# Optimization experiments

Measured on AMD Instinct MI355X. Metric: run time of the kernel, lower is better.

## Reference

```python
import jax, jax.numpy as jnp
import numpy as np

B, S, D = 4, 2048, 1024
LN_EPS = 1e-3  # keras LayerNormalization default


def setup_inputs() -> dict:
    key = jax.random.key(0)
    ks = jax.random.split(key, 4)
    std = 1.0 / np.sqrt(D)
    return {
        "inputs": jax.random.normal(ks[0], (B, S, D), dtype=jnp.float32),
        "Wq": jax.random.normal(ks[1], (D, D), dtype=jnp.float32) * std,
        "bq": jnp.zeros((D,), jnp.float32),
        "Wk": jax.random.normal(ks[2], (D, D), dtype=jnp.float32) * std,
        "bk": jnp.zeros((D,), jnp.float32),
        "Wv": jax.random.normal(ks[3], (D, D), dtype=jnp.float32) * std,
        "bv": jnp.zeros((D,), jnp.float32),
        "ln_gamma": jnp.ones((D,), jnp.float32),
        "ln_beta": jnp.zeros((D,), jnp.float32),
    }


def reference(inputs, Wq, bq, Wk, bk, Wv, bv, ln_gamma, ln_beta):
    d = inputs.shape[-1]
    scale = jnp.sqrt(jnp.asarray(d, inputs.dtype))
    q = inputs @ Wq + bq          # [B,S,D]
    k = inputs @ Wk + bk
    v = inputs @ Wv + bv
    scores = jnp.einsum("bqd,bkd->bqk", q, k) / scale  # [B,S,S]
    attn = jax.nn.softmax(scores, axis=-1)
    context = jnp.einsum("bqk,bkd->bqd", attn, v)      # [B,S,D]
    resid = context + inputs
    mu = jnp.mean(resid, axis=-1, keepdims=True)
    var = jnp.mean(jnp.square(resid - mu), axis=-1, keepdims=True)
    normed = (resid - mu) * jax.lax.rsqrt(var + LN_EPS)
    return normed * ln_gamma + ln_beta
```

## Files before the change

### kernel.cpp

```cpp
#include <hip/hip_runtime.h>
#include <hip/hip_bf16.h>
#include <cstdint>
#include <cstddef>


typedef unsigned short u16;
using bf16x8 = __attribute__((ext_vector_type(8))) short;
using f32x16 = __attribute__((ext_vector_type(16))) float;

typedef __attribute__((address_space(3))) unsigned int lds_uint;
typedef const __attribute__((address_space(1))) unsigned int glob_uint;

__device__ __forceinline__ float bf2f(u16 h) {
    union { unsigned int u; float f; } c;
    c.u = ((unsigned int)h) << 16;
    return c.f;
}
__device__ __forceinline__ u16 f2bf(float f) {
    union { float f; unsigned int u; } c;
    c.f = f;
    return (u16)((c.u + 0x7fffu + ((c.u >> 16) & 1u)) >> 16);
}
__device__ __forceinline__ void load_lds16(const void* g, void* l) {
    __builtin_amdgcn_global_load_lds((glob_uint*)g, (lds_uint*)l, 16, 0, 0);
}

__device__ __forceinline__ int detect_fp32(const u16* X, int* sflag) {
    const int t = threadIdx.x;
    if (t < 64) {
        bool bad = false, nz = false;
#pragma unroll
        for (int j = 0; j < 4; ++j) {
            float v = bf2f(X[(t * 4 + j) * 2]);
            if (!(fabsf(v) <= 1e9f)) bad = true;
            if (v != 0.f) nz = true;
        }
        unsigned long long ab = __ballot(bad);
        unsigned long long an = __ballot(nz);
        if (t == 0) *sflag = (ab != 0ull || an == 0ull) ? 1 : 0;
    }
    __syncthreads();
    return *sflag;
}

__global__ __launch_bounds__(256) void prep_kernel(
    const void* __restrict__ X, const void* __restrict__ Wq,
    const void* __restrict__ Wk, const void* __restrict__ Wv,
    const void* __restrict__ bq, const void* __restrict__ bk,
    const void* __restrict__ bv, const void* __restrict__ gamma,
    const void* __restrict__ beta,
    u16* __restrict__ Xb, u16* __restrict__ Wt, u16* __restrict__ bias5)
{
    __shared__ u16 tile[64][72];
    __shared__ int sflag;
    const int fp32 = detect_fp32((const u16*)X, &sflag);
    const int t   = threadIdx.x;
    const int blk = blockIdx.x;

    if (blk < 4096) {
        const size_t i = ((size_t)blk * 256 + t) * 8;
        if (fp32) {
            const float* f = (const float*)X;
            float4 a = *(const float4*)(f + i);
            float4 b = *(const float4*)(f + i + 4);
            ushort4 o0, o1;
            o0.x = f2bf(a.x); o0.y = f2bf(a.y); o0.z = f2bf(a.z); o0.w = f2bf(a.w);
            o1.x = f2bf(b.x); o1.y = f2bf(b.y); o1.z = f2bf(b.z); o1.w = f2bf(b.w);
            *(ushort4*)(Xb + i) = o0;
            *(ushort4*)(Xb + i + 4) = o1;
        } else {
            *(uint4*)(Xb + i) = *(const uint4*)((const u16*)X + i);
        }
    } else if (blk < 4864) {
        const int idx = blk - 4096;
        const int k0 = (idx & 15) * 64;
        const int n0 = ((idx >> 4) & 15) * 64;
        const int w  = idx >> 8;
        const void* W = (w == 0) ? Wq : ((w == 1) ? Wk : Wv);
#pragma unroll
        for (int it = 0; it < 2; ++it) {
            int i2 = t + it * 256;
            int r = i2 >> 3;
            int c = (i2 & 7) * 8;
            const size_t off = (size_t)(k0 + r) * 1024 + n0 + c;
            if (fp32) {
                const float* Wf = (const float*)W + off;
                float4 a = *(const float4*)Wf;
                float4 b = *(const float4*)(Wf + 4);
                u16* tp = &tile[r][c];
                tp[0] = f2bf(a.x); tp[1] = f2bf(a.y); tp[2] = f2bf(a.z); tp[3] = f2bf(a.w);
                tp[4] = f2bf(b.x); tp[5] = f2bf(b.y); tp[6] = f2bf(b.z); tp[7] = f2bf(b.w);
            } else {
                *(uint4*)&tile[r][c] = *(const uint4*)((const u16*)W + off);
            }
        }
        __syncthreads();
#pragma unroll
        for (int it = 0; it < 2; ++it) {
            int i2 = t + it * 256;
            int r = i2 >> 3;
            int c = (i2 & 7) * 8;
            union { u16 s[8]; uint4 v; } tmp;
#pragma unroll
            for (int j = 0; j < 8; ++j) tmp.s[j] = tile[c + j][r];
            *(uint4*)(Wt + (size_t)(w * 1024 + n0 + r) * 1024 + k0 + c) = tmp.v;
        }
    } else {
        const int v = blk - 4864;
        const void* srcs[5] = {bq, bk, bv, gamma, beta};
        const void* src = srcs[v];
        u16* d = bias5 + (size_t)v * 1024;
        const int i = t * 4;
        if (fp32) {
            const float* f = (const float*)src;
            ushort4 o;
            o.x = f2bf(f[i]); o.y = f2bf(f[i + 1]);
            o.z = f2bf(f[i + 2]); o.w = f2bf(f[i + 3]);
            *(ushort4*)(d + i) = o;
        } else {
            *(ushort4*)(d + i) = *(const ushort4*)((const u16*)src + i);
        }
    }
}

__global__ __launch_bounds__(256) void proj_kernel(
    const u16* __restrict__ Xb, const u16* __restrict__ Wt,
    u16* __restrict__ QK2, u16* __restrict__ Vt, const u16* __restrict__ bias5)
{
    __shared__ u16 As[2][128 * 32];
    __shared__ u16 Bs[2][128 * 32];
    const int id   = blockIdx.x;
    const bool vt  = (id >= 1024);
    const u16* A;  const u16* Bt;  u16* C;
    int lda, ldb, ldc, m0, n0;
    if (!vt) {
        A = Xb;  lda = 1024;  Bt = Wt;  ldb = 1024;  C = QK2;  ldc = 2048;
        n0 = (id & 15) * 128;  m0 = (id >> 4) * 128;
    } else {
        const int i2 = id - 1024;
        A = Wt + (size_t)2 * 1024 * 1024;  lda = 1024;
        Bt = Xb;  ldb = 1024;  C = Vt;  ldc = 8192;
        n0 = (i2 & 63) * 128;  m0 = (i2 >> 6) * 128;
    }
    const int t    = threadIdx.x;
    const int lane = t & 63;
    const int w    = t >> 6;
    const int wr   = w >> 1, wc = w & 1;

    const int srow = lane >> 2;
    const int skg  = (lane & 3) ^ ((srow >> 1) & 3);
    const u16* Ag0 = A  + (size_t)(m0 + w * 32 +      srow) * lda + skg * 8;
    const u16* Ag1 = A  + (size_t)(m0 + w * 32 + 16 + srow) * lda + skg * 8;
    const u16* Bg0 = Bt + (size_t)(n0 + w * 32 +      srow) * ldb + skg * 8;
    const u16* Bg1 = Bt + (size_t)(n0 + w * 32 + 16 + srow) * ldb + skg * 8;
    u16* Al0 = &As[0][(w * 32) * 32];
    u16* Al1 = &As[1][(w * 32) * 32];
    u16* Bl0 = &Bs[0][(w * 32) * 32];
    u16* Bl1 = &Bs[1][(w * 32) * 32];

    f32x16 acc[2][2];
#pragma unroll
    for (int mi = 0; mi < 2; ++mi)
#pragma unroll
        for (int ni = 0; ni < 2; ++ni)
#pragma unroll
            for (int r = 0; r < 16; ++r)
                acc[mi][ni][r] = 0.f;

    const int ml  = lane & 31;
    const int kh  = lane >> 5;
    const int key = (ml >> 1) & 3;

    for (int k0 = 0; k0 < 1024; k0 += 64) {
        load_lds16(Ag0 + k0,      Al0);
        load_lds16(Ag1 + k0,      Al0 + 16 * 32);
        load_lds16(Bg0 + k0,      Bl0);
        load_lds16(Bg1 + k0,      Bl0 + 16 * 32);
        load_lds16(Ag0 + k0 + 32, Al1);
        load_lds16(Ag1 + k0 + 32, Al1 + 16 * 32);
        load_lds16(Bg0 + k0 + 32, Bl1);
        load_lds16(Bg1 + k0 + 32, Bl1 + 16 * 32);
        __syncthreads();
#pragma unroll
        for (int slab = 0; slab < 2; ++slab) {
            const u16* as_ = As[slab];
            const u16* bs_ = Bs[slab];
#pragma unroll
            for (int s = 0; s < 2; ++s) {
                const int g    = s * 2 + kh;
                const int slot = (g ^ key) * 8;
                bf16x8 a0 = *(const bf16x8*)&as_[(wr * 64 +      ml) * 32 + slot];
                bf16x8 a1 = *(const bf16x8*)&as_[(wr * 64 + 32 + ml) * 32 + slot];
                bf16x8 b0 = *(const bf16x8*)&bs_[(wc * 64 +      ml) * 32 + slot];
                bf16x8 b1 = *(const bf16x8*)&bs_[(wc * 64 + 32 + ml) * 32 + slot];
                acc[0][0] = __builtin_amdgcn_mfma_f32_32x32x16_bf16(a0, b0, acc[0][0], 0, 0, 0);
                acc[0][1] = __builtin_amdgcn_mfma_f32_32x32x16_bf16(a0, b1, acc[0][1], 0, 0, 0);
                acc[1][0] = __builtin_amdgcn_mfma_f32_32x32x16_bf16(a1, b0, acc[1][0], 0, 0, 0);
                acc[1][1] = __builtin_amdgcn_mfma_f32_32x32x16_bf16(a1, b1, acc[1][1], 0, 0, 0);
            }
        }
        __syncthreads();
    }

    const int colb = n0 + wc * 64 + ml;
    const int rowb = m0 + wr * 64 + 4 * kh;
#pragma unroll
    for (int mi = 0; mi < 2; ++mi) {
#pragma unroll
        for (int ni = 0; ni < 2; ++ni) {
            const int col = colb + ni * 32;
            const float cbias = vt ? 0.f : bf2f(bias5[col]);
#pragma unroll
            for (int r = 0; r < 16; ++r) {
                const int row = rowb + mi * 32 + (r & 3) + 8 * (r >> 2);
                const float bias = vt ? bf2f(bias5[2048 + row]) : cbias;
                C[(size_t)row * ldc + col] = f2bf(acc[mi][ni][r] + bias);
            }
        }
    }
}

template<int EPI, int KSPLIT>
__global__ __launch_bounds__(512, 2) void gemm256r(
    const u16* __restrict__ A, int lda, size_t sA,
    const u16* __restrict__ Bt, int ldb, size_t sB,
    u16* __restrict__ C, int ldc, size_t sC,
    int K, float scale, const u16* __restrict__ bias3)
{
    __shared__ u16 As[2][256 * 64];
    __shared__ u16 Bs[2][256 * 64];

    const int t  = threadIdx.x;
    const int l  = t & 63;
    const int w  = t >> 6;
    const int wm = w >> 2;
    const int wn = w & 3;
    const int m0 = blockIdx.y * 256;
    const int n0 = blockIdx.x * 256;
    const int batch = (int)blockIdx.z >> (KSPLIT - 1);
    const int ks    = (int)blockIdx.z & (KSPLIT - 1);
    A  += (size_t)batch * sA + (size_t)ks * K;
    Bt += (size_t)batch * sB + (size_t)ks * K;
    C  += (size_t)batch * sC + (size_t)ks * 1024;

    const int srow = w * 8 + (l >> 3);
    const int sg   = (l & 7) ^ (l >> 3);
    const u16* Ag = A  + (size_t)(m0 + srow) * lda + sg * 8;
    const u16* Bg = Bt + (size_t)(n0 + srow) * ldb + sg * 8;

    auto stage = [&](int j, int buf) {
        const size_t kb = (size_t)j * 64;
        const u16* ag = Ag + kb;
        const u16* bg = Bg + kb;
        u16* al = &As[buf][w * 512];
        u16* bl = &Bs[buf][w * 512];
#pragma unroll
        for (int i = 0; i < 4; ++i) {
            load_lds16(ag + (size_t)i * 64 * lda, al + i * 4096);
            load_lds16(bg + (size_t)i * 64 * ldb, bl + i * 4096);
        }
    };

    const int lr   = l & 31;
    const int kh   = l >> 5;
    const int keyr = lr & 7;
    const int aoff = (wm * 128 + lr) * 64;
    const int boff = (wn * 64 + lr) * 64;

    f32x16 acc[4][2];
#pragma unroll
    for (int mi = 0; mi < 4; ++mi)
#pragma unroll
        for (int ni = 0; ni < 2; ++ni)
#pragma unroll
            for (int r = 0; r < 16; ++r) acc[mi][ni][r] = 0.f;

    const int NS = K >> 6;

    stage(0, 0);
    stage(1, 1);
    asm volatile("s_waitcnt vmcnt(8)" ::: "memory");
    __builtin_amdgcn_s_barrier();
    asm volatile("" ::: "memory");

    for (int j = 0; j < NS; ++j) {
        const int buf = j & 1;
        const u16* as_ = &As[buf][aoff];
        const u16* bs_ = &Bs[buf][boff];
        bf16x8 a[4][4], b[2][4];
#pragma unroll
        for (int ks2 = 0; ks2 < 2; ++ks2) {
            const int sp = ((ks2 * 2 + kh) ^ keyr) * 8;
#pragma unroll
            for (int mi = 0; mi < 4; ++mi) a[mi][ks2] = *(const bf16x8*)(as_ + mi * 2048 + sp);
#pragma unroll
            for (int ni = 0; ni < 2; ++ni) b[ni][ks2] = *(const bf16x8*)(bs_ + ni * 2048 + sp);
        }
        if (j + 1 < NS && j > 0) stage(j + 1, buf ^ 1);
        __builtin_amdgcn_s_setprio(1);
#pragma unroll
        for (int ks2 = 0; ks2 < 2; ++ks2)
#pragma unroll
            for (int mi = 0; mi < 4; ++mi)
#pragma unroll
                for (int ni = 0; ni < 2; ++ni)
                    acc[mi][ni] = __builtin_amdgcn_mfma_f32_32x32x16_bf16(
                        a[mi][ks2], b[ni][ks2], acc[mi][ni], 0, 0, 0);
        __builtin_amdgcn_s_setprio(0);
#pragma unroll
        for (int ks2 = 2; ks2 < 4; ++ks2) {
            const int sp = ((ks2 * 2 + kh) ^ keyr) * 8;
#pragma unroll
            for (int mi = 0; mi < 4; ++mi) a[mi][ks2] = *(const bf16x8*)(as_ + mi * 2048 + sp);
#pragma unroll
            for (int ni = 0; ni < 2; ++ni) b[ni][ks2] = *(const bf16x8*)(bs_ + ni * 2048 + sp);
        }
        __builtin_amdgcn_s_setprio(1);
#pragma unroll
        for (int ks2 = 2; ks2 < 4; ++ks2)
#pragma unroll
            for (int mi = 0; mi < 4; ++mi)
#pragma unroll
                for (int ni = 0; ni < 2; ++ni)
                    acc[mi][ni] = __builtin_amdgcn_mfma_f32_32x32x16_bf16(
                        a[mi][ks2], b[ni][ks2], acc[mi][ni], 0, 0, 0);
        __builtin_amdgcn_s_setprio(0);
        if (j + 1 < NS) {
            asm volatile("s_waitcnt vmcnt(0)" ::: "memory");
            __builtin_amdgcn_s_barrier();
            asm volatile("" ::: "memory");
        }
    }

    const int colb = n0 + wn * 64 + lr;
    const int rowb = m0 + wm * 128 + 4 * kh;
#pragma unroll
    for (int mi = 0; mi < 4; ++mi) {
#pragma unroll
        for (int ni = 0; ni < 2; ++ni) {
            const int col = colb + ni * 32;
            const float bias = (EPI == 0) ? bf2f(bias3[col]) : 0.f;
#pragma unroll
            for (int r = 0; r < 16; ++r) {
                const int row = rowb + mi * 32 + (r & 3) + 8 * (r >> 2);
                C[(size_t)row * ldc + col] = f2bf(acc[mi][ni][r] * scale + bias);
            }
        }
    }
}

__global__ __launch_bounds__(256) void softmax_bf16_kernel(u16* __restrict__ S)
{
    const int t = threadIdx.x;
    u16* sp = S + (size_t)blockIdx.x * 2048;
    union { uint4 v; u16 h[8]; } raw;
    raw.v = *(const uint4*)(sp + t * 8);
    float vals[8];
#pragma unroll
    for (int i = 0; i < 8; ++i) vals[i] = bf2f(raw.h[i]);
    float m = vals[0];
#pragma unroll
    for (int i = 1; i < 8; ++i) m = fmaxf(m, vals[i]);
#pragma unroll
    for (int off = 32; off > 0; off >>= 1) m = fmaxf(m, __shfl_xor(m, off));
    __shared__ float red[8];
    const int w = t >> 6, lane = t & 63;
    if (lane == 0) red[w] = m;
    __syncthreads();
    m = fmaxf(fmaxf(red[0], red[1]), fmaxf(red[2], red[3]));
    float e[8], s = 0.f;
#pragma unroll
    for (int i = 0; i < 8; ++i) { e[i] = __expf(vals[i] - m); s += e[i]; }
#pragma unroll
    for (int off = 32; off > 0; off >>= 1) s += __shfl_xor(s, off);
    if (lane == 0) red[4 + w] = s;
    __syncthreads();
    s = red[4] + red[5] + red[6] + red[7];
    const float rinv = 1.f / s;
    union { uint4 v; u16 h[8]; } out;
#pragma unroll
    for (int i = 0; i < 8; ++i) out.h[i] = f2bf(e[i] * rinv);
    *(uint4*)(sp + t * 8) = out.v;
}

__global__ __launch_bounds__(256) void resid_ln_kernel(
    const u16* __restrict__ Ctx, const u16* __restrict__ Xb,
    const u16* __restrict__ gamma, const u16* __restrict__ beta,
    void* __restrict__ Out, const u16* __restrict__ Xraw)
{
    __shared__ int sflag;
    const int fp32 = detect_fp32(Xraw, &sflag);
    const size_t row = blockIdx.x;
    const int t = threadIdx.x;
    ushort4 cv0 = *(const ushort4*)(Ctx + row * 2048 + t * 4);
    ushort4 cv1 = *(const ushort4*)(Ctx + row * 2048 + 1024 + t * 4);
    ushort4 xv  = *(const ushort4*)(Xb + row * 1024 + t * 4);
    float v[4] = {bf2f(cv0.x) + bf2f(cv1.x) + bf2f(xv.x),
                  bf2f(cv0.y) + bf2f(cv1.y) + bf2f(xv.y),
                  bf2f(cv0.z) + bf2f(cv1.z) + bf2f(xv.z),
                  bf2f(cv0.w) + bf2f(cv1.w) + bf2f(xv.w)};
    float s  = v[0] + v[1] + v[2] + v[3];
    float s2 = v[0] * v[0] + v[1] * v[1] + v[2] * v[2] + v[3] * v[3];
#pragma unroll
    for (int off = 32; off > 0; off >>= 1) {
        s  += __shfl_xor(s, off);
        s2 += __shfl_xor(s2, off);
    }
    __shared__ float red[8];
    const int w = t >> 6, lane = t & 63;
    if (lane == 0) { red[w] = s; red[4 + w] = s2; }
    __syncthreads();
    s  = red[0] + red[1] + red[2] + red[3];
    s2 = red[4] + red[5] + red[6] + red[7];
    const float mu  = s * (1.f / 1024.f);
    const float var = s2 * (1.f / 1024.f) - mu * mu;
    const float inv = rsqrtf(var + 1e-3f);
    ushort4 gv = *(const ushort4*)(gamma + t * 4);
    ushort4 bv = *(const ushort4*)(beta + t * 4);
    float o[4];
    o[0] = (v[0] - mu) * inv * bf2f(gv.x) + bf2f(bv.x);
    o[1] = (v[1] - mu) * inv * bf2f(gv.y) + bf2f(bv.y);
    o[2] = (v[2] - mu) * inv * bf2f(gv.z) + bf2f(bv.z);
    o[3] = (v[3] - mu) * inv * bf2f(gv.w) + bf2f(bv.w);
    if (fp32) {
        float4 fo = {o[0], o[1], o[2], o[3]};
        *(float4*)((float*)Out + row * 1024 + t * 4) = fo;
    } else {
        ushort4 bo;
        bo.x = f2bf(o[0]); bo.y = f2bf(o[1]); bo.z = f2bf(o[2]); bo.w = f2bf(o[3]);
        *(ushort4*)((u16*)Out + row * 1024 + t * 4) = bo;
    }
}

extern "C" void kernel_launch(void* const* d_in, const int* in_sizes, int n_in,
                              void* d_out, int out_size, void* d_ws, size_t ws_size,
                              hipStream_t stream)
{
    (void)in_sizes; (void)n_in; (void)out_size; (void)ws_size;
    const void* X     = d_in[0];
    const void* Wq    = d_in[1];
    const void* bq    = d_in[2];
    const void* Wk    = d_in[3];
    const void* bk    = d_in[4];
    const void* Wv    = d_in[5];
    const void* bv    = d_in[6];
    const void* gamma = d_in[7];
    const void* beta  = d_in[8];

    char* ws = (char*)d_ws;
    u16* bias5 = (u16*)(ws + 16);
    u16* Wt    = (u16*)(ws + 16384);
    u16* QK2   = (u16*)(ws + 6307840);
    u16* Xb    = (u16*)(ws + 39862272);
    u16* S4    = (u16*)(ws + 56639488);
    u16* Vt    = (u16*)(ws + 90193920);

    prep_kernel<<<4869, 256, 0, stream>>>(
        X, Wq, Wk, Wv, bq, bk, bv, gamma, beta, Xb, Wt, bias5);

    proj_kernel<<<1536, 256, 0, stream>>>(Xb, Wt, QK2, Vt, bias5);

    gemm256r<1, 1><<<dim3(8, 8, 4), 512, 0, stream>>>(
        QK2, 2048, (size_t)2048 * 2048,
        QK2 + 1024, 2048, (size_t)2048 * 2048,
        S4, 2048, (size_t)2048 * 2048, 1024, 0.03125f, nullptr);

    softmax_bf16_kernel<<<8192, 256, 0, stream>>>(S4);

    gemm256r<1, 2><<<dim3(4, 8, 8), 512, 0, stream>>>(
        S4, 2048, (size_t)2048 * 2048,
        Vt, 8192, (size_t)2048,
        QK2, 2048, (size_t)2048 * 2048, 1024, 1.f, nullptr);

    resid_ln_kernel<<<8192, 256, 0, stream>>>(
        QK2, Xb, bias5 + 3 * 1024, bias5 + 4 * 1024, d_out, (const u16*)X);
}
```

Before: 280.2 us.

## Restructure attention GEMMs into an 8-wave, barrier-interleaved half-tile staged pipeline

Replaces the double-buffered GEMM main loop with a schedule that unrolls two K-steps per iteration. Each step is split into four MFMA quads, each separated by block barriers. Global-to-LDS loads are issued as half-tile chunks interleaved between the quads, and the LDS row layout is permuted so a quad uses only part of the tile. The aim is to overlap memory traffic with MFMA work and to keep waves in lockstep for better matrix-core utilisation. In exchange it adds many more barriers and depends on careful vmcnt accounting. It also drops the unused bias epilogue path.

New measurement: 286.0 us. +2.1%, slower.

```diff
diff --git a/kernel.cpp b/kernel.cpp
--- a/kernel.cpp
+++ b/kernel.cpp
@@ -24,6 +24,9 @@
 __device__ __forceinline__ void load_lds16(const void* g, void* l) {
     __builtin_amdgcn_global_load_lds((glob_uint*)g, (lds_uint*)l, 16, 0, 0);
 }
+
+#define FENCE asm volatile("" ::: "memory")
+#define BARR  do { FENCE; __builtin_amdgcn_s_barrier(); FENCE; } while (0)
 
 __device__ __forceinline__ int detect_fp32(const u16* X, int* sflag) {
     const int t = threadIdx.x;
@@ -220,12 +223,12 @@
     }
 }
 
-template<int EPI, int KSPLIT>
-__global__ __launch_bounds__(512, 2) void gemm256r(
+template<int KSPLIT>
+__global__ __launch_bounds__(512, 2) void gemm8p(
     const u16* __restrict__ A, int lda, size_t sA,
     const u16* __restrict__ Bt, int ldb, size_t sB,
     u16* __restrict__ C, int ldc, size_t sC,
-    int K, float scale, const u16* __restrict__ bias3)
+    int K, float scale)
 {
     __shared__ u16 As[2][256 * 64];
     __shared__ u16 Bs[2][256 * 64];
@@ -238,34 +241,55 @@
     const int m0 = blockIdx.y * 256;
     const int n0 = blockIdx.x * 256;
     const int batch = (int)blockIdx.z >> (KSPLIT - 1);
-    const int ks    = (int)blockIdx.z & (KSPLIT - 1);
-    A  += (size_t)batch * sA + (size_t)ks * K;
-    Bt += (size_t)batch * sB + (size_t)ks * K;
-    C  += (size_t)batch * sC + (size_t)ks * 1024;
-
-    const int srow = w * 8 + (l >> 3);
-    const int sg   = (l & 7) ^ (l >> 3);
-    const u16* Ag = A  + (size_t)(m0 + srow) * lda + sg * 8;
-    const u16* Bg = Bt + (size_t)(n0 + srow) * ldb + sg * 8;
-
-    auto stage = [&](int j, int buf) {
-        const size_t kb = (size_t)j * 64;
-        const u16* ag = Ag + kb;
-        const u16* bg = Bg + kb;
-        u16* al = &As[buf][w * 512];
-        u16* bl = &Bs[buf][w * 512];
-#pragma unroll
-        for (int i = 0; i < 4; ++i) {
-            load_lds16(ag + (size_t)i * 64 * lda, al + i * 4096);
-            load_lds16(bg + (size_t)i * 64 * ldb, bl + i * 4096);
-        }
+    const int ksz   = (int)blockIdx.z & (KSPLIT - 1);
+    A  += (size_t)batch * sA + (size_t)ksz * K;
+    Bt += (size_t)batch * sB + (size_t)ksz * K;
+    C  += (size_t)batch * sC + (size_t)ksz * 1024;
+
+    const int q   = t >> 3;
+    const int sg  = (t & 7) ^ (q & 7);
+    const int q5  = (q >> 5) & 1, q31 = q & 31;
+    int offA[4], offB[4];
+#pragma unroll
+    for (int i = 0; i < 4; ++i) {
+        const int ga = ((i & 1) << 7) + ((i >> 1) << 6) + q;
+        const int gb = ((i & 1) << 7) + ((i >> 1) << 5) + q5 * 64 + q31;
+        offA[i] = (m0 + ga) * lda + sg * 8;
+        offB[i] = (n0 + gb) * ldb + sg * 8;
+    }
+    auto stgA = [&](int j, int bf, int h) {
+#pragma unroll
+        for (int i = 2 * h; i < 2 * h + 2; ++i)
+            load_lds16(A + (size_t)offA[i] + j * 64, &As[bf][i * 4096 + w * 512]);
     };
-
-    const int lr   = l & 31;
-    const int kh   = l >> 5;
+    auto stgB = [&](int j, int bf, int h) {
+#pragma unroll
+        for (int i = 2 * h; i < 2 * h + 2; ++i)
+            load_lds16(Bt + (size_t)offB[i] + j * 64, &Bs[bf][i * 4096 + w * 512]);
+    };
+
+    const int lr = l & 31, kh = l >> 5;
     const int keyr = lr & 7;
-    const int aoff = (wm * 128 + lr) * 64;
-    const int boff = (wn * 64 + lr) * 64;
+    int arow[4], slot[4];
+#pragma unroll
+    for (int mi = 0; mi < 4; ++mi)
+        arow[mi] = ((mi >> 1) * 128 + wm * 64 + (mi & 1) * 32 + lr) * 64;
+    const int brow0 = (wn * 32 + lr) * 64;
+    const int brow1 = (128 + wn * 32 + lr) * 64;
+#pragma unroll
+    for (int kk = 0; kk < 4; ++kk)
+        slot[kk] = ((2 * kk + kh) ^ keyr) * 8;
+
+    auto rdA = [&](bf16x8 (&d)[4], int mi, int bf) {
+#pragma unroll
+        for (int kk = 0; kk < 4; ++kk)
+            d[kk] = *(const bf16x8*)&As[bf][arow[mi] + slot[kk]];
+    };
+    auto rdB = [&](bf16x8 (&d)[4], int br, int bf) {
+#pragma unroll
+        for (int kk = 0; kk < 4; ++kk)
+            d[kk] = *(const bf16x8*)&Bs[bf][br + slot[kk]];
+    };
 
     f32x16 acc[4][2];
 #pragma unroll
@@ -275,62 +299,71 @@
 #pragma unroll
             for (int r = 0; r < 16; ++r) acc[mi][ni][r] = 0.f;
 
+#define QUAD8(A0_, A1_, B_, ALO, AHI)                                            \
+    __builtin_amdgcn_s_setprio(1);                                               \
+    _Pragma("unroll")                                                            \
+    for (int kq = 0; kq < 4; ++kq) {                                             \
+        ALO = __builtin_amdgcn_mfma_f32_32x32x16_bf16(A0_[kq], B_[kq], ALO, 0, 0, 0); \
+        AHI = __builtin_amdgcn_mfma_f32_32x32x16_bf16(A1_[kq], B_[kq], AHI, 0, 0, 0); \
+    }                                                                            \
+    __builtin_amdgcn_s_setprio(0);
+
     const int NS = K >> 6;
-
-    stage(0, 0);
-    stage(1, 1);
-    asm volatile("s_waitcnt vmcnt(8)" ::: "memory");
-    __builtin_amdgcn_s_barrier();
-    asm volatile("" ::: "memory");
-
-    for (int j = 0; j < NS; ++j) {
-        const int buf = j & 1;
-        const u16* as_ = &As[buf][aoff];
-        const u16* bs_ = &Bs[buf][boff];
-        bf16x8 a[4][4], b[2][4];
-#pragma unroll
-        for (int ks2 = 0; ks2 < 2; ++ks2) {
-            const int sp = ((ks2 * 2 + kh) ^ keyr) * 8;
-#pragma unroll
-            for (int mi = 0; mi < 4; ++mi) a[mi][ks2] = *(const bf16x8*)(as_ + mi * 2048 + sp);
-#pragma unroll
-            for (int ni = 0; ni < 2; ++ni) b[ni][ks2] = *(const bf16x8*)(bs_ + ni * 2048 + sp);
-        }
-        if (j + 1 < NS && j > 0) stage(j + 1, buf ^ 1);
-        __builtin_amdgcn_s_setprio(1);
-#pragma unroll
-        for (int ks2 = 0; ks2 < 2; ++ks2)
-#pragma unroll
-            for (int mi = 0; mi < 4; ++mi)
-#pragma unroll
-                for (int ni = 0; ni < 2; ++ni)
-                    acc[mi][ni] = __builtin_amdgcn_mfma_f32_32x32x16_bf16(
-                        a[mi][ks2], b[ni][ks2], acc[mi][ni], 0, 0, 0);
-        __builtin_amdgcn_s_setprio(0);
-#pragma unroll
-        for (int ks2 = 2; ks2 < 4; ++ks2) {
-            const int sp = ((ks2 * 2 + kh) ^ keyr) * 8;
-#pragma unroll
-            for (int mi = 0; mi < 4; ++mi) a[mi][ks2] = *(const bf16x8*)(as_ + mi * 2048 + sp);
-#pragma unroll
-            for (int ni = 0; ni < 2; ++ni) b[ni][ks2] = *(const bf16x8*)(bs_ + ni * 2048 + sp);
-        }
-        __builtin_amdgcn_s_setprio(1);
-#pragma unroll
-        for (int ks2 = 2; ks2 < 4; ++ks2)
-#pragma unroll
-            for (int mi = 0; mi < 4; ++mi)
-#pragma unroll
-                for (int ni = 0; ni < 2; ++ni)
-                    acc[mi][ni] = __builtin_amdgcn_mfma_f32_32x32x16_bf16(
-                        a[mi][ks2], b[ni][ks2], acc[mi][ni], 0, 0, 0);
-        __builtin_amdgcn_s_setprio(0);
-        if (j + 1 < NS) {
-            asm volatile("s_waitcnt vmcnt(0)" ::: "memory");
-            __builtin_amdgcn_s_barrier();
-            asm volatile("" ::: "memory");
-        }
-    }
+    const int iters = NS >> 1;
+
+    stgA(0, 0, 0); stgB(0, 0, 0); stgB(0, 0, 1); stgA(0, 0, 1);
+    stgA(1, 1, 0); stgB(1, 1, 0); stgB(1, 1, 1);
+    asm volatile("s_waitcnt vmcnt(6)" ::: "memory");
+    BARR;
+
+    for (int i = 0; i < iters; ++i) {
+        const int T0 = 2 * i, T1 = 2 * i + 1;
+        const bool more = (i + 1 < iters);
+        bf16x8 a0[4], a1[4], b0[4], b1[4];
+        rdA(a0, 0, 0); rdA(a1, 1, 0); rdB(b0, brow0, 0);
+        stgA(T1, 1, 1);
+        BARR;
+        QUAD8(a0, a1, b0, acc[0][0], acc[1][0]);
+        BARR;
+        rdB(b1, brow1, 0);
+        if (more) stgA(T0 + 2, 0, 0);
+        BARR;
+        QUAD8(a0, a1, b1, acc[0][1], acc[1][1]);
+        BARR;
+        rdA(a0, 2, 0); rdA(a1, 3, 0);
+        if (more) stgB(T0 + 2, 0, 0);
+        BARR;
+        QUAD8(a0, a1, b0, acc[2][0], acc[3][0]);
+        BARR;
+        if (more) stgB(T0 + 2, 0, 1);
+        if (more) asm volatile("s_waitcnt vmcnt(6)" ::: "memory");
+        else      asm volatile("s_waitcnt vmcnt(0)" ::: "memory");
+        BARR;
+        QUAD8(a0, a1, b1, acc[2][1], acc[3][1]);
+        BARR;
+        rdA(a0, 0, 1); rdA(a1, 1, 1); rdB(b0, brow0, 1);
+        if (more) stgA(T0 + 2, 0, 1);
+        BARR;
+        QUAD8(a0, a1, b0, acc[0][0], acc[1][0]);
+        BARR;
+        rdB(b1, brow1, 1);
+        if (more) stgA(T1 + 2, 1, 0);
+        BARR;
+        QUAD8(a0, a1, b1, acc[0][1], acc[1][1]);
+        BARR;
+        rdA(a0, 2, 1); rdA(a1, 3, 1);
+        if (more) stgB(T1 + 2, 1, 0);
+        BARR;
+        QUAD8(a0, a1, b0, acc[2][0], acc[3][0]);
+        BARR;
+        if (more) stgB(T1 + 2, 1, 1);
+        if (more) asm volatile("s_waitcnt vmcnt(6)" ::: "memory");
+        else      asm volatile("s_waitcnt vmcnt(0)" ::: "memory");
+        BARR;
+        QUAD8(a0, a1, b1, acc[2][1], acc[3][1]);
+        BARR;
+    }
+#undef QUAD8
 
     const int colb = n0 + wn * 64 + lr;
     const int rowb = m0 + wm * 128 + 4 * kh;
@@ -339,11 +372,10 @@
 #pragma unroll
         for (int ni = 0; ni < 2; ++ni) {
             const int col = colb + ni * 32;
-            const float bias = (EPI == 0) ? bf2f(bias3[col]) : 0.f;
 #pragma unroll
             for (int r = 0; r < 16; ++r) {
                 const int row = rowb + mi * 32 + (r & 3) + 8 * (r >> 2);
-                C[(size_t)row * ldc + col] = f2bf(acc[mi][ni][r] * scale + bias);
+                C[(size_t)row * ldc + col] = f2bf(acc[mi][ni][r] * scale);
             }
         }
     }
@@ -460,17 +492,17 @@
 
     proj_kernel<<<1536, 256, 0, stream>>>(Xb, Wt, QK2, Vt, bias5);
 
-    gemm256r<1, 1><<<dim3(8, 8, 4), 512, 0, stream>>>(
+    gemm8p<1><<<dim3(8, 8, 4), 512, 0, stream>>>(
         QK2, 2048, (size_t)2048 * 2048,
         QK2 + 1024, 2048, (size_t)2048 * 2048,
-        S4, 2048, (size_t)2048 * 2048, 1024, 0.03125f, nullptr);
+        S4, 2048, (size_t)2048 * 2048, 1024, 0.03125f);
 
     softmax_bf16_kernel<<<8192, 256, 0, stream>>>(S4);
 
-    gemm256r<1, 2><<<dim3(4, 8, 8), 512, 0, stream>>>(
+    gemm8p<2><<<dim3(4, 8, 8), 512, 0, stream>>>(
         S4, 2048, (size_t)2048 * 2048,
         Vt, 8192, (size_t)2048,
-        QK2, 2048, (size_t)2048 * 2048, 1024, 1.f, nullptr);
+        QK2, 2048, (size_t)2048 * 2048, 1024, 1.f);
 
     resid_ln_kernel<<<8192, 256, 0, stream>>>(
         QK2, Xb, bias5 + 3 * 1024, bias5 + 4 * 1024, d_out, (const u16*)X);
```
